# Performance work log

Measured on AMD Instinct MI355X. Metric: run time of the kernel, lower is better.

## Reference

```python
import jax, jax.numpy as jnp
import numpy as np

INPUT_HW = (800, 1024)
STRIDE = 16
HS, WS = INPUT_HW[0] // STRIDE, INPUT_HW[1] // STRIDE  # 50, 64
FG_T, BG_T = 0.7, 0.3
POS_FRAC = 0.5
BATCH_PER_IMG = 256
POS_CAP = int(BATCH_PER_IMG * POS_FRAC)  # 128
# config.anchors: 3 scales x 3 ratios, (w, h) in pixels
_scales = np.array([128.0, 256.0, 512.0])
_ratios = np.array([0.5, 1.0, 2.0])
ANCHOR_WH = np.stack([np.array([s * np.sqrt(r), s / np.sqrt(r)])
                      for s in _scales for r in _ratios], axis=0).astype(np.float32)  # [9,2]
A = ANCHOR_WH.shape[0]
N = HS * WS * A


def build_anchors():
    """Normalized x1y1x2y2 anchors, invalid (out-of-image) anchors zeroed. [N,4]"""
    gx, gy = np.meshgrid(np.arange(WS), np.arange(HS))            # [HS,WS]
    center = (np.stack([gx, gy], -1).astype(np.float32) + 0.5) * STRIDE  # [HS,WS,2]
    center = center[:, :, None, :]                                 # [HS,WS,1,2]
    wh_img = np.array([WS * STRIDE, HS * STRIDE], np.float32)      # (1024, 800)
    a = ANCHOR_WH[None, None, :, :]
    x1y1 = (center - a / 2.0) / wh_img                             # [HS,WS,A,2]
    x2y2 = (center + a / 2.0) / wh_img
    valid = ((x1y1[..., 0] > 0) & (x1y1[..., 1] > 0) &
             (x2y2[..., 0] < 1) & (x2y2[..., 1] < 1)).astype(np.float32)
    boxes = np.concatenate([x1y1, x2y2], -1) * valid[..., None]
    return jnp.asarray(boxes.reshape(N, 4))


def cal_iou(anchors, gt):  # anchors [N,4], gt [M,4] -> [N,M]
    a = anchors[:, None, :]
    g = gt[None, :, :]
    mins = jnp.maximum(a[..., :2], g[..., :2])
    maxs = jnp.minimum(a[..., 2:], g[..., 2:])
    wh = jnp.maximum(maxs - mins, 0.0)
    inter = wh[..., 0] * wh[..., 1]
    area_a = (a[..., 2] - a[..., 0]) * (a[..., 3] - a[..., 1])
    area_g = (g[..., 2] - g[..., 0]) * (g[..., 3] - g[..., 1])
    return inter / (area_a + area_g - inter + 1e-7)


def encode_offset(gt, ref):  # [N,4], [N,4] -> [N,4] tx,ty,tw,th
    w_gt = gt[:, 2] - gt[:, 0]
    h_gt = gt[:, 3] - gt[:, 1]
    xc_gt = (gt[:, 2] + gt[:, 0]) / 2
    yc_gt = (gt[:, 3] + gt[:, 1]) / 2
    w_r = ref[:, 2] - ref[:, 0]
    h_r = ref[:, 3] - ref[:, 1]
    xc_r = (ref[:, 2] + ref[:, 0]) / 2
    yc_r = (ref[:, 3] + ref[:, 1]) / 2
    w_rs = jnp.where(w_r > 0, w_r, 1.0)  # guard zeroed (invalid) anchors
    h_rs = jnp.where(h_r > 0, h_r, 1.0)
    tx = jnp.where(w_gt > 0, (xc_gt - xc_r) / w_rs, 0.0)
    ty = jnp.where(h_gt > 0, (yc_gt - yc_r) / h_rs, 0.0)
    tw = jnp.where(w_gt > 0, jnp.log(jnp.where(w_gt > 0, w_gt / w_rs, 1.0)), 0.0)
    th = jnp.where(h_gt > 0, jnp.log(jnp.where(h_gt > 0, h_gt / h_rs, 1.0)), 0.0)
    return jnp.stack([tx, ty, tw, th], -1)


def _per_image(gt, key, anchors):
    iou = cal_iou(anchors, gt)                    # [N,M]
    matched_iou = iou.max(axis=-1)                # [N]
    matched_idx = iou.argmax(axis=-1)             # [N]
    best_iou = iou.max(axis=0)                    # [M]
    best_idx = iou.argmax(axis=0)                 # [M]
    # positive candidates: high-IoU anchors + per-gt best-matching anchors
    forced = jnp.zeros((N,), jnp.float32).at[best_idx].max(
        jnp.where(best_iou > 0, 1.0, 0.0))
    pos_cand = (matched_iou > FG_T) | (forced > 0)
    neg_cand = matched_iou < BG_T
    n_pos = jnp.minimum(pos_cand.sum(), POS_CAP)
    n_neg = BATCH_PER_IMG - n_pos
    k1, k2 = jax.random.split(key)
    # random subsampling: random priority + rank threshold == random_shuffle[:n]
    rp = jnp.where(pos_cand, jax.random.uniform(k1, (N,)), -1.0)
    rank_p = jnp.argsort(jnp.argsort(-rp))
    sel_pos = pos_cand & (rank_p < n_pos)
    rn = jnp.where(neg_cand, jax.random.uniform(k2, (N,)), -1.0)
    rank_n = jnp.argsort(jnp.argsort(-rn))
    sel_neg = neg_cand & (rank_n < n_neg)
    # offsets for sampled positives against their matched gt
    offsets = encode_offset(gt[matched_idx], anchors)          # [N,4]
    offsets = offsets * sel_pos[:, None].astype(offsets.dtype)
    cls = -jnp.ones((N,), jnp.float32)
    cls = jnp.where(sel_pos, 1.0, cls)
    cls = jnp.where(sel_neg, 0.0, cls)  # neg overwrites, as in the original
    return jnp.concatenate([cls[:, None], offsets], axis=-1)   # [N,5]


def setup_inputs() -> dict:
    key = jax.random.key(0)
    B, M, C = 16, 64, 20
    k1, k2, k3 = jax.random.split(key, 3)
    xy1 = jax.random.uniform(k1, (B, M, 2)) * 0.7
    wh = jax.random.uniform(k2, (B, M, 2)) * 0.25 + 0.02
    boxes = jnp.concatenate([xy1, jnp.minimum(xy1 + wh, 1.0)], axis=-1)
    cls_part = jax.random.uniform(k3, (B, M, C + 1))
    x = jnp.concatenate([cls_part, boxes], axis=-1).astype(jnp.float32)  # [B,M,25]
    return {"x": x}


def reference(x) -> jnp.ndarray:
    gt = x[..., -4:]                      # [B,M,4]
    B = gt.shape[0]
    anchors = build_anchors()             # [N,4]
    keys = jax.random.split(jax.random.key(42), B)
    out = jax.vmap(lambda g, k: _per_image(g, k, anchors))(gt, keys)  # [B,N,5]
    return out.reshape(B, HS, WS, A, 1 + 4)
```

## Files before the change

### kernel.cpp

```cpp
#include <hip/hip_runtime.h>
#include <stdint.h>
#include <math.h>

typedef unsigned int u32;
typedef unsigned long long u64;

#define NN_ 28800
#define MM_ 64
#define BB_ 16
#define XROW_ 25
#define POS_CAP_ 128u
#define BATCH_ 256u
#define NBLK_ 75
#define XSPAN_ 1579

struct Keys { u32 k[BB_][4]; };

__host__ __device__ __forceinline__ u32 rotl32(u32 v, u32 r){ return (v<<r)|(v>>(32u-r)); }

__host__ __device__ __forceinline__ void tf2x32(u32 k0, u32 k1, u32 x0, u32 x1, u32& y0, u32& y1){
  u32 ks2 = k0 ^ k1 ^ 0x1BD11BDAu;
  x0 += k0; x1 += k1;
#define TFR(r) { x0 += x1; x1 = rotl32(x1,(r)); x1 ^= x0; }
  TFR(13) TFR(15) TFR(26) TFR(6)   x0 += k1;  x1 += ks2 + 1u;
  TFR(17) TFR(29) TFR(16) TFR(24)  x0 += ks2; x1 += k0  + 2u;
  TFR(13) TFR(15) TFR(26) TFR(6)   x0 += k0;  x1 += k1  + 3u;
  TFR(17) TFR(29) TFR(16) TFR(24)  x0 += k1;  x1 += ks2 + 4u;
  TFR(13) TFR(15) TFR(26) TFR(6)   x0 += ks2; x1 += k0  + 5u;
#undef TFR
  y0 = x0; y1 = x1;
}

__device__ __forceinline__ void anchor_from(int a, int cell,
                                            float& ox1, float& oy1, float& ox2, float& oy2){
  #pragma clang fp contract(off)
  int w = cell & 63;
  int h = cell >> 6;
  int p = (a >= 6) ? 2 : ((a >= 3) ? 1 : 0);
  int q = a - p*3;
  float sf = (p==0) ? 128.0f : ((p==1) ? 256.0f : 512.0f);
  const float SQH = 0.70710678118654752440f;
  const float SQ2 = 1.41421356237309514547f;
  float cw = (q==0) ? SQH : ((q==1) ? 1.0f : SQ2);
  float ch = (q==0) ? SQ2 : ((q==1) ? 1.0f : SQH);
  float hx = (sf*cw) * 0.5f;
  float hy = (sf*ch) * 0.5f;
  float cx = ((float)w + 0.5f) * 16.0f;
  float cy = ((float)h + 0.5f) * 16.0f;
  float X1 = (cx - hx) / 1024.0f;
  float Y1 = (cy - hy) / 800.0f;
  float X2 = (cx + hx) / 1024.0f;
  float Y2 = (cy + hy) / 800.0f;
  bool valid = (X1 > 0.0f) && (Y1 > 0.0f) && (X2 < 1.0f) && (Y2 < 1.0f);
  ox1 = valid ? X1 : 0.0f;
  oy1 = valid ? Y1 : 0.0f;
  ox2 = valid ? X2 : 0.0f;
  oy2 = valid ? Y2 : 0.0f;
}

__device__ __forceinline__ float rdlane(float v, int k){
  return __int_as_float(__builtin_amdgcn_readlane(__float_as_int(v), k));
}

__device__ __forceinline__ float iou_of(float bx1,float by1,float bx2,float by2,float ba,
                                        float gx1,float gy1,float gx2,float gy2,float garea){
  #pragma clang fp contract(off)
  float ix1 = fmaxf(bx1,gx1), iy1 = fmaxf(by1,gy1);
  float ix2 = fminf(bx2,gx2), iy2 = fminf(by2,gy2);
  float iw = fmaxf(ix2-ix1, 0.0f), ih = fmaxf(iy2-iy1, 0.0f);
  float inter = iw*ih;
  float den = ba + garea;
  den = den - inter;
  den = den + 1e-7f;
  return inter / den;
}

__global__ __launch_bounds__(384) void k_main(const float* __restrict__ x, Keys keys,
                                              u64* __restrict__ bestpart,
                                              u32* __restrict__ cnts_part,
                                              u32* __restrict__ rpv, u32* __restrict__ rnv){
  #pragma clang fp contract(off)
  int tid = threadIdx.x;
  int lane = tid & 63;
  int wid = tid >> 6;
  int bx = blockIdx.x;
  int b = blockIdx.y;
  int cbase = (bx*6 + wid)*64;

  __shared__ float xr[XSPAN_];
  for (int t = tid; t < XSPAN_; t += 384) xr[t] = x[b*(MM_*XROW_) + 21 + t];
  __syncthreads();

  float gx1 = xr[25*lane+0], gy1 = xr[25*lane+1], gx2 = xr[25*lane+2], gy2 = xr[25*lane+3];
  float garea = (gx2-gx1)*(gy2-gy1);

  int ia = cbase + lane;
  int a = ia % 9, cell = ia / 9;
  float ax1,ay1,ax2,ay2;
  anchor_from(a, cell, ax1,ay1,ax2,ay2);
  float aarea = (ax2-ax1)*(ay2-ay1);

  u64 valid_mask = __ballot(ax2 > 0.0f);
  u64 pcbits = 0;
  u64 ncbits = ~valid_mask;
  u64 bk = 0;

  u64 vm = valid_mask;
  while (vm){
    int k1 = __ffsll((unsigned long long)vm) - 1; vm &= vm - 1ull;
    int k2 = vm ? __ffsll((unsigned long long)vm) - 1 : k1; vm &= vm - 1ull;
    int k3 = vm ? __ffsll((unsigned long long)vm) - 1 : k1; vm &= vm - 1ull;
    int k4 = vm ? __ffsll((unsigned long long)vm) - 1 : k1; vm &= vm - 1ull;
    float c1x1=rdlane(ax1,k1), c1y1=rdlane(ay1,k1), c1x2=rdlane(ax2,k1), c1y2=rdlane(ay2,k1), c1a=rdlane(aarea,k1);
    float c2x1=rdlane(ax1,k2), c2y1=rdlane(ay1,k2), c2x2=rdlane(ax2,k2), c2y2=rdlane(ay2,k2), c2a=rdlane(aarea,k2);
    float c3x1=rdlane(ax1,k3), c3y1=rdlane(ay1,k3), c3x2=rdlane(ax2,k3), c3y2=rdlane(ay2,k3), c3a=rdlane(aarea,k3);
    float c4x1=rdlane(ax1,k4), c4y1=rdlane(ay1,k4), c4x2=rdlane(ax2,k4), c4y2=rdlane(ay2,k4), c4a=rdlane(aarea,k4);
    float i1 = iou_of(c1x1,c1y1,c1x2,c1y2,c1a, gx1,gy1,gx2,gy2,garea);
    float i2 = iou_of(c2x1,c2y1,c2x2,c2y2,c2a, gx1,gy1,gx2,gy2,garea);
    float i3 = iou_of(c3x1,c3y1,c3x2,c3y2,c3a, gx1,gy1,gx2,gy2,garea);
    float i4 = iou_of(c4x1,c4y1,c4x2,c4y2,c4a, gx1,gy1,gx2,gy2,garea);
    u64 p1 = __ballot(i1 > 0.7f), n1 = __ballot(i1 >= 0.3f);
    u64 p2 = __ballot(i2 > 0.7f), n2 = __ballot(i2 >= 0.3f);
    u64 p3 = __ballot(i3 > 0.7f), n3 = __ballot(i3 >= 0.3f);
    u64 p4 = __ballot(i4 > 0.7f), n4 = __ballot(i4 >= 0.3f);
    if (p1)  pcbits |= 1ull << k1;
    if (!n1) ncbits |= 1ull << k1;
    if (p2)  pcbits |= 1ull << k2;
    if (!n2) ncbits |= 1ull << k2;
    if (p3)  pcbits |= 1ull << k3;
    if (!n3) ncbits |= 1ull << k3;
    if (p4)  pcbits |= 1ull << k4;
    if (!n4) ncbits |= 1ull << k4;
    u32 q1 = __float_as_uint(i1), q2 = __float_as_uint(i2);
    u32 q3 = __float_as_uint(i3), q4 = __float_as_uint(i4);
    u64 key1 = ((u64)q1 << 32) | (u64)(0xFFFFFFFFu - (u32)(cbase + k1));
    u64 key2 = ((u64)q2 << 32) | (u64)(0xFFFFFFFFu - (u32)(cbase + k2));
    u64 key3 = ((u64)q3 << 32) | (u64)(0xFFFFFFFFu - (u32)(cbase + k3));
    u64 key4 = ((u64)q4 << 32) | (u64)(0xFFFFFFFFu - (u32)(cbase + k4));
    if (q1 && key1 > bk) bk = key1;
    if (q2 && key2 > bk) bk = key2;
    if (q3 && key3 > bk) bk = key3;
    if (q4 && key4 > bk) bk = key4;
  }

  int i = cbase + lane;
  bool pc = (pcbits >> lane) & 1ull;
  bool nc = (ncbits >> lane) & 1ull;
  u32 rp = 0, rn = 0;
  if (pcbits){
    u32 a0,a1;
    tf2x32(keys.k[b][0], keys.k[b][1], 0u, (u32)i, a0,a1);
    rp = pc ? ((a0^a1) >> 9) + 1u : 0u;
  }
  if (ncbits){
    u32 c0,c1;
    tf2x32(keys.k[b][2], keys.k[b][3], 0u, (u32)i, c0,c1);
    rn = nc ? ((c0^c1) >> 9) + 1u : 0u;
  }
  rpv[b*NN_+i] = rp;
  rnv[b*NN_+i] = rn;

  __shared__ u64 wl[384];
  __shared__ u32 scnt[12];
  wl[wid*64 + lane] = bk;
  if (lane == 0){
    scnt[wid*2+0] = (u32)__popcll(pcbits);
    scnt[wid*2+1] = (u32)__popcll(ncbits);
  }
  __syncthreads();
  if (tid < 64){
    u64 m = wl[tid];
    #pragma unroll
    for (int w = 1; w < 6; ++w){ u64 v = wl[w*64+tid]; if (v > m) m = v; }
    bestpart[((size_t)(b*NBLK_ + bx))*64 + tid] = m;
  }
  if (tid == 0){
    u32 c0 = 0, c1 = 0;
    #pragma unroll
    for (int w = 0; w < 6; ++w){ c0 += scnt[w*2+0]; c1 += scnt[w*2+1]; }
    cnts_part[(b*NBLK_ + bx)*2 + 0] = c0;
    cnts_part[(b*NBLK_ + bx)*2 + 1] = c1;
  }
}

__global__ __launch_bounds__(1024) void k_selfix(const float* __restrict__ x,
                                                 const u64* __restrict__ bestpart,
                                                 const u32* __restrict__ cnts_part,
                                                 Keys keys,
                                                 u32* __restrict__ rpv,
                                                 const u32* __restrict__ rnv,
                                                 u32* __restrict__ selp){
  #pragma clang fp contract(off)
  int cls = blockIdx.x, b = blockIdx.y, tid = threadIdx.x;
  int lane = tid & 63, wid = tid >> 6;
  int id = b*2 + cls;

  __shared__ float gbox[MM_][4];
  __shared__ float ga[MM_];
  __shared__ u64 red[16][64];
  __shared__ u32 scp[16], scn[16];
  __shared__ u32 fist[64];
  __shared__ float fmx[16][64];
  __shared__ u32 sq[4];
  __shared__ u32 hist[4096];
  __shared__ u32 wt[16], wsuf[16];
  __shared__ u32 bc[2];
  __shared__ u64 L[512];
  __shared__ u32 lc;

  if (tid < 256) gbox[tid>>2][tid&3] = x[(b*MM_ + (tid>>2))*XROW_ + 21 + (tid&3)];
  __syncthreads();
  if (tid < MM_){
    float g0=gbox[tid][0], g1=gbox[tid][1], g2=gbox[tid][2], g3=gbox[tid][3];
    ga[tid] = (g2-g0)*(g3-g1);
  }

  u64 m = 0;
  for (int blk = wid; blk < NBLK_; blk += 16){
    u64 v = bestpart[((size_t)(b*NBLK_ + blk))*64 + lane];
    if (v > m) m = v;
  }
  red[wid][lane] = m;

  u32 cp = 0, cn = 0;
  if (tid < NBLK_){ cp = cnts_part[(b*NBLK_+tid)*2+0]; cn = cnts_part[(b*NBLK_+tid)*2+1]; }
  #pragma unroll
  for (int off = 32; off >= 1; off >>= 1){
    cp += (u32)__shfl_xor((int)cp, off, 64);
    cn += (u32)__shfl_xor((int)cn, off, 64);
  }
  if (lane == 0){ scp[wid] = cp; scn[wid] = cn; }
  __syncthreads();

  if (tid < 64){
    u64 mm = red[0][tid];
    #pragma unroll
    for (int w = 1; w < 16; ++w){ u64 v = red[w][tid]; if (v > mm) mm = v; }
    fist[tid] = ((u32)(mm >> 32) != 0u) ? (0xFFFFFFFFu - (u32)mm) : 0xFFFFFFFFu;
  }
  if (tid == 0){
    u32 c0 = 0, c1 = 0;
    for (int w = 0; w < 16; ++w){ c0 += scp[w]; c1 += scn[w]; }
    sq[0] = c0; sq[1] = c1;
  }
  __syncthreads();

  {
    int j = tid & 63, q = tid >> 6;
    float mm = 0.0f;
    u32 fi = fist[j];
    if (fi != 0xFFFFFFFFu){
      float ax1,ay1,ax2,ay2;
      anchor_from((int)(fi % 9), (int)(fi / 9), ax1,ay1,ax2,ay2);
      float aarea = (ax2-ax1)*(ay2-ay1);
      #pragma unroll
      for (int t = 0; t < 4; ++t){
        int j2 = q*4 + t;
        float iou = iou_of(ax1,ay1,ax2,ay2,aarea,
                           gbox[j2][0],gbox[j2][1],gbox[j2][2],gbox[j2][3], ga[j2]);
        mm = fmaxf(mm, iou);
      }
    }
    fmx[q][j] = mm;
  }
  __syncthreads();

  if (tid < 64){
    int j = tid;
    u32 fi = fist[j];
    bool valid = (fi != 0xFFFFFFFFu);
    float mm = fmx[0][j];
    #pragma unroll
    for (int q = 1; q < 16; ++q) mm = fmaxf(mm, fmx[q][j]);
    bool wasc = (mm > 0.7f);
    bool first = true;
    for (int j2 = 0; j2 < j; ++j2) if (fist[j2] == fi) first = false;
    bool add = valid && !wasc && first;
    u64 bal = __ballot(add);
    if (cls == 0 && valid){
      u32 a0,a1; tf2x32(keys.k[b][0], keys.k[b][1], 0u, fi, a0,a1);
      rpv[(size_t)b*NN_ + fi] = ((a0^a1) >> 9) + 1u;
    }
    if (tid == 0) sq[2] = sq[0] + (u32)__popcll(bal);
  }
  __syncthreads();

  u32 posc = sq[2], negc = sq[1];
  u32 npos = min(posc, POS_CAP_);
  u32 K   = cls ? (BATCH_ - npos) : npos;
  u32 cnt = cls ? negc : posc;
  if (cnt <= K){
    if (tid == 0){ selp[id*2+0] = 0u; selp[id*2+1] = 0xFFFFFFFFu; }
    return;
  }

  const u32* v = (cls ? rnv : rpv) + (size_t)b*NN_;
  const uint4* v4 = (const uint4*)v;
  #pragma unroll
  for (int h = 0; h < 4; ++h) hist[h*1024 + tid] = 0;
  if (tid == 0) lc = 0;
  __syncthreads();
  for (int i2 = tid; i2 < NN_/4; i2 += 1024){
    uint4 q = v4[i2];
    if (q.x) atomicAdd(&hist[(q.x-1u)>>11], 1u);
    if (q.y) atomicAdd(&hist[(q.y-1u)>>11], 1u);
    if (q.z) atomicAdd(&hist[(q.z-1u)>>11], 1u);
    if (q.w) atomicAdd(&hist[(q.w-1u)>>11], 1u);
  }
  __syncthreads();
  u32 s = hist[tid*4+0] + hist[tid*4+1] + hist[tid*4+2] + hist[tid*4+3];
  u32 incl = s;
  #pragma unroll
  for (int off = 1; off < 64; off <<= 1){
    u32 o = (u32)__shfl_down((int)incl, off, 64);
    incl += (lane + off < 64) ? o : 0u;
  }
  if (lane == 0) wt[wid] = incl;
  __syncthreads();
  if (tid < 16){ u32 ss = 0; for (int w = tid+1; w < 16; ++w) ss += wt[w]; wsuf[tid] = ss; }
  __syncthreads();
  u32 excl = incl - s + wsuf[wid];
  if (excl < K && excl + s >= K){
    u32 acc = excl;
    for (int q = 3; q >= 0; --q){
      u32 h = hist[tid*4 + q];
      if (acc + h >= K){ bc[0] = (u32)(tid*4 + q); bc[1] = K - acc; break; }
      acc += h;
    }
  }
  __syncthreads();
  u32 B = bc[0], Kp = bc[1];
  for (int i2 = tid; i2 < NN_/4; i2 += 1024){
    uint4 q = v4[i2];
    #pragma unroll
    for (int c = 0; c < 4; ++c){
      u32 xv = (c==0)?q.x:(c==1)?q.y:(c==2)?q.z:q.w;
      if (xv && ((xv - 1u) >> 11) == B){
        u32 p = atomicAdd(&lc, 1u);
        if (p < 512u) L[p] = ((u64)xv << 32) | (u32)(i2*4 + c);
      }
    }
  }
  __syncthreads();
  u32 n = min(lc, 512u);
  if (tid < (int)n){
    u64 me = L[tid]; u32 mv = (u32)(me >> 32), mi = (u32)me;
    u32 r = 0;
    for (u32 t2 = 0; t2 < n; ++t2){
      u64 o = L[t2]; u32 ov = (u32)(o >> 32), oi = (u32)o;
      r += (ov > mv) || (ov == mv && oi < mi);
    }
    if (r == Kp - 1u){ selp[id*2+0] = mv; selp[id*2+1] = mi; }
  }
}

__global__ __launch_bounds__(256) void k_out(const float* __restrict__ x,
                                             const u32* __restrict__ rpv,
                                             const u32* __restrict__ rnv,
                                             const u32* __restrict__ selp,
                                             float* __restrict__ out){
  #pragma clang fp contract(off)
  int b = blockIdx.y, tid = threadIdx.x;
  __shared__ float xr[XSPAN_];
  for (int t = tid; t < XSPAN_; t += 256) xr[t] = x[b*(MM_*XROW_) + 21 + t];
  __syncthreads();
  int i = blockIdx.x*256 + tid;
  if (i >= NN_) return;

  u32 pth = selp[(b*2+0)*2+0], pcut = selp[(b*2+0)*2+1];
  u32 nth = selp[(b*2+1)*2+0], ncut = selp[(b*2+1)*2+1];
  u32 pv = rpv[b*NN_+i], nv = rnv[b*NN_+i];
  bool selpos = (pv > 0u) && (pv > pth || (pv == pth && (u32)i <= pcut));
  bool selneg = (nv > 0u) && (nv > nth || (nv == nth && (u32)i <= ncut));
  float cls = selpos ? 1.0f : -1.0f;
  if (selneg) cls = 0.0f;

  float tx = 0.0f, ty = 0.0f, tw = 0.0f, th = 0.0f;
  if (selpos){
    int a = i % 9, cell = i / 9;
    float ax1,ay1,ax2,ay2;
    anchor_from(a, cell, ax1,ay1,ax2,ay2);
    float area_a = (ax2-ax1)*(ay2-ay1);
    float best = -1.0f; int bj = 0;
    for (int j = 0; j < MM_; ++j){
      float g0=xr[25*j+0], g1=xr[25*j+1], g2=xr[25*j+2], g3=xr[25*j+3];
      float ix1 = fmaxf(ax1,g0), iy1 = fmaxf(ay1,g1);
      float ix2 = fminf(ax2,g2), iy2 = fminf(ay2,g3);
      float iw = fmaxf(ix2-ix1, 0.0f), ih = fmaxf(iy2-iy1, 0.0f);
      float inter = iw*ih;
      float den = area_a + (g2-g0)*(g3-g1);
      den = den - inter;
      den = den + 1e-7f;
      float iou = inter / den;
      if (iou > best){ best = iou; bj = j; }
    }
    float g0=xr[25*bj+0], g1=xr[25*bj+1], g2=xr[25*bj+2], g3=xr[25*bj+3];
    float wgt = g2-g0, hgt = g3-g1;
    float xcg = (g2+g0)*0.5f, ycg = (g3+g1)*0.5f;
    float wr = ax2-ax1, hr = ay2-ay1;
    float xcr = (ax2+ax1)*0.5f, ycr = (ay2+ay1)*0.5f;
    float wrs = (wr > 0.0f) ? wr : 1.0f;
    float hrs = (hr > 0.0f) ? hr : 1.0f;
    tx = (wgt > 0.0f) ? (xcg - xcr)/wrs : 0.0f;
    ty = (hgt > 0.0f) ? (ycg - ycr)/hrs : 0.0f;
    tw = (wgt > 0.0f) ? logf(wgt/wrs) : 0.0f;
    th = (hgt > 0.0f) ? logf(hgt/hrs) : 0.0f;
  }
  float* o = out + (size_t)(b*NN_+i)*5;
  o[0] = cls; o[1] = tx; o[2] = ty; o[3] = tw; o[4] = th;
}

extern "C" void kernel_launch(void* const* d_in, const int* in_sizes, int n_in,
                              void* d_out, int out_size, void* d_ws, size_t ws_size,
                              hipStream_t stream) {
  const float* x = (const float*)d_in[0];
  float* out = (float*)d_out;
  char* ws = (char*)d_ws;

  u32* selp      = (u32*)(ws + 0);
  u64* bestpart  = (u64*)(ws + 512);
  u32* cnts_part = (u32*)(ws + 614912);
  u32* rpv       = (u32*)(ws + 624640);
  u32* rnv       = (u32*)(ws + 2467840);
  (void)ws_size; (void)in_sizes; (void)n_in; (void)out_size;

  Keys keys;
  for (int b = 0; b < BB_; ++b){
    u32 r0, r1;
    tf2x32(0u, 42u, 0u, (u32)b, r0, r1);
    tf2x32(r0, r1, 0u, 0u, keys.k[b][0], keys.k[b][1]);
    tf2x32(r0, r1, 0u, 1u, keys.k[b][2], keys.k[b][3]);
  }

  k_main  <<<dim3(NBLK_, BB_), 384, 0, stream>>>(x, keys, bestpart, cnts_part, rpv, rnv);
  k_selfix<<<dim3(2, BB_), 1024, 0, stream>>>(x, bestpart, cnts_part, keys, rpv, rnv, selp);
  k_out   <<<dim3(113, BB_), 256, 0, stream>>>(x, rpv, rnv, selp, out);
}
```

Before: 71.14 us.

## Restructure anchor IoU pass into valid-row blocks with row-level early skip

The main kernel now splits its work into two kinds of blocks. Sixteen blocks per image walk only the valid anchor rows, grouped per anchor shape, using per-shape geometry ranges computed on the host. A wave skips the whole row when no ground-truth box overlaps it vertically. The other blocks only fill in random values for invalid anchors and count them. This removes the per-anchor readlane broadcasts and any IoU work on invalid anchors, and it shrinks the best-key reduction in k_selfix. The cost is load imbalance across the row blocks and more complex indexing.

```diff
diff --git a/kernel.cpp b/kernel.cpp
--- a/kernel.cpp
+++ b/kernel.cpp
@@ -11,10 +11,13 @@
 #define XROW_ 25
 #define POS_CAP_ 128u
 #define BATCH_ 256u
-#define NBLK_ 75
 #define XSPAN_ 1579
+#define RBLK_ 16
+#define FBLK_ 75
+#define NPART_ (RBLK_ + FBLK_)
 
 struct Keys { u32 k[BB_][4]; };
+struct Geo  { int wlo[9], wspan[9], hlo[9], rowbase[10]; float hxv[9], hyv[9]; };
 
 __host__ __device__ __forceinline__ u32 rotl32(u32 v, u32 r){ return (v<<r)|(v>>(32u-r)); }
 
@@ -31,11 +34,7 @@
   y0 = x0; y1 = x1;
 }
 
-__device__ __forceinline__ void anchor_from(int a, int cell,
-                                            float& ox1, float& oy1, float& ox2, float& oy2){
-  #pragma clang fp contract(off)
-  int w = cell & 63;
-  int h = cell >> 6;
+__host__ __device__ __forceinline__ void anchor_hxy(int a, float& hx, float& hy){
   int p = (a >= 6) ? 2 : ((a >= 3) ? 1 : 0);
   int q = a - p*3;
   float sf = (p==0) ? 128.0f : ((p==1) ? 256.0f : 512.0f);
@@ -43,8 +42,16 @@
   const float SQ2 = 1.41421356237309514547f;
   float cw = (q==0) ? SQH : ((q==1) ? 1.0f : SQ2);
   float ch = (q==0) ? SQ2 : ((q==1) ? 1.0f : SQH);
-  float hx = (sf*cw) * 0.5f;
-  float hy = (sf*ch) * 0.5f;
+  hx = (sf*cw) * 0.5f;
+  hy = (sf*ch) * 0.5f;
+}
+
+__device__ __forceinline__ void anchor_from(int a, int cell,
+                                            float& ox1, float& oy1, float& ox2, float& oy2){
+  #pragma clang fp contract(off)
+  int w = cell & 63;
+  int h = cell >> 6;
+  float hx, hy; anchor_hxy(a, hx, hy);
   float cx = ((float)w + 0.5f) * 16.0f;
   float cy = ((float)h + 0.5f) * 16.0f;
   float X1 = (cx - hx) / 1024.0f;
@@ -58,10 +65,6 @@
   oy2 = valid ? Y2 : 0.0f;
 }
 
-__device__ __forceinline__ float rdlane(float v, int k){
-  return __int_as_float(__builtin_amdgcn_readlane(__float_as_int(v), k));
-}
-
 __device__ __forceinline__ float iou_of(float bx1,float by1,float bx2,float by2,float ba,
                                         float gx1,float gy1,float gx2,float gy2,float garea){
   #pragma clang fp contract(off)
@@ -75,7 +78,7 @@
   return inter / den;
 }
 
-__global__ __launch_bounds__(384) void k_main(const float* __restrict__ x, Keys keys,
+__global__ __launch_bounds__(384) void k_main(const float* __restrict__ x, Keys keys, Geo geo,
                                               u64* __restrict__ bestpart,
                                               u32* __restrict__ cnts_part,
                                               u32* __restrict__ rpv, u32* __restrict__ rnv){
@@ -85,101 +88,121 @@
   int wid = tid >> 6;
   int bx = blockIdx.x;
   int b = blockIdx.y;
-  int cbase = (bx*6 + wid)*64;
-
-  __shared__ float xr[XSPAN_];
-  for (int t = tid; t < XSPAN_; t += 384) xr[t] = x[b*(MM_*XROW_) + 21 + t];
-  __syncthreads();
-
-  float gx1 = xr[25*lane+0], gy1 = xr[25*lane+1], gx2 = xr[25*lane+2], gy2 = xr[25*lane+3];
-  float garea = (gx2-gx1)*(gy2-gy1);
-
-  int ia = cbase + lane;
-  int a = ia % 9, cell = ia / 9;
-  float ax1,ay1,ax2,ay2;
-  anchor_from(a, cell, ax1,ay1,ax2,ay2);
-  float aarea = (ax2-ax1)*(ay2-ay1);
-
-  u64 valid_mask = __ballot(ax2 > 0.0f);
-  u64 pcbits = 0;
-  u64 ncbits = ~valid_mask;
-  u64 bk = 0;
-
-  u64 vm = valid_mask;
-  while (vm){
-    int k1 = __ffsll((unsigned long long)vm) - 1; vm &= vm - 1ull;
-    int k2 = vm ? __ffsll((unsigned long long)vm) - 1 : k1; vm &= vm - 1ull;
-    int k3 = vm ? __ffsll((unsigned long long)vm) - 1 : k1; vm &= vm - 1ull;
-    int k4 = vm ? __ffsll((unsigned long long)vm) - 1 : k1; vm &= vm - 1ull;
-    float c1x1=rdlane(ax1,k1), c1y1=rdlane(ay1,k1), c1x2=rdlane(ax2,k1), c1y2=rdlane(ay2,k1), c1a=rdlane(aarea,k1);
-    float c2x1=rdlane(ax1,k2), c2y1=rdlane(ay1,k2), c2x2=rdlane(ax2,k2), c2y2=rdlane(ay2,k2), c2a=rdlane(aarea,k2);
-    float c3x1=rdlane(ax1,k3), c3y1=rdlane(ay1,k3), c3x2=rdlane(ax2,k3), c3y2=rdlane(ay2,k3), c3a=rdlane(aarea,k3);
-    float c4x1=rdlane(ax1,k4), c4y1=rdlane(ay1,k4), c4x2=rdlane(ax2,k4), c4y2=rdlane(ay2,k4), c4a=rdlane(aarea,k4);
-    float i1 = iou_of(c1x1,c1y1,c1x2,c1y2,c1a, gx1,gy1,gx2,gy2,garea);
-    float i2 = iou_of(c2x1,c2y1,c2x2,c2y2,c2a, gx1,gy1,gx2,gy2,garea);
-    float i3 = iou_of(c3x1,c3y1,c3x2,c3y2,c3a, gx1,gy1,gx2,gy2,garea);
-    float i4 = iou_of(c4x1,c4y1,c4x2,c4y2,c4a, gx1,gy1,gx2,gy2,garea);
-    u64 p1 = __ballot(i1 > 0.7f), n1 = __ballot(i1 >= 0.3f);
-    u64 p2 = __ballot(i2 > 0.7f), n2 = __ballot(i2 >= 0.3f);
-    u64 p3 = __ballot(i3 > 0.7f), n3 = __ballot(i3 >= 0.3f);
-    u64 p4 = __ballot(i4 > 0.7f), n4 = __ballot(i4 >= 0.3f);
-    if (p1)  pcbits |= 1ull << k1;
-    if (!n1) ncbits |= 1ull << k1;
-    if (p2)  pcbits |= 1ull << k2;
-    if (!n2) ncbits |= 1ull << k2;
-    if (p3)  pcbits |= 1ull << k3;
-    if (!n3) ncbits |= 1ull << k3;
-    if (p4)  pcbits |= 1ull << k4;
-    if (!n4) ncbits |= 1ull << k4;
-    u32 q1 = __float_as_uint(i1), q2 = __float_as_uint(i2);
-    u32 q3 = __float_as_uint(i3), q4 = __float_as_uint(i4);
-    u64 key1 = ((u64)q1 << 32) | (u64)(0xFFFFFFFFu - (u32)(cbase + k1));
-    u64 key2 = ((u64)q2 << 32) | (u64)(0xFFFFFFFFu - (u32)(cbase + k2));
-    u64 key3 = ((u64)q3 << 32) | (u64)(0xFFFFFFFFu - (u32)(cbase + k3));
-    u64 key4 = ((u64)q4 << 32) | (u64)(0xFFFFFFFFu - (u32)(cbase + k4));
-    if (q1 && key1 > bk) bk = key1;
-    if (q2 && key2 > bk) bk = key2;
-    if (q3 && key3 > bk) bk = key3;
-    if (q4 && key4 > bk) bk = key4;
-  }
-
-  int i = cbase + lane;
-  bool pc = (pcbits >> lane) & 1ull;
-  bool nc = (ncbits >> lane) & 1ull;
-  u32 rp = 0, rn = 0;
-  if (pcbits){
-    u32 a0,a1;
-    tf2x32(keys.k[b][0], keys.k[b][1], 0u, (u32)i, a0,a1);
-    rp = pc ? ((a0^a1) >> 9) + 1u : 0u;
-  }
-  if (ncbits){
-    u32 c0,c1;
-    tf2x32(keys.k[b][2], keys.k[b][3], 0u, (u32)i, c0,c1);
-    rn = nc ? ((c0^c1) >> 9) + 1u : 0u;
-  }
-  rpv[b*NN_+i] = rp;
-  rnv[b*NN_+i] = rn;
-
-  __shared__ u64 wl[384];
-  __shared__ u32 scnt[12];
-  wl[wid*64 + lane] = bk;
-  if (lane == 0){
-    scnt[wid*2+0] = (u32)__popcll(pcbits);
-    scnt[wid*2+1] = (u32)__popcll(ncbits);
-  }
-  __syncthreads();
-  if (tid < 64){
-    u64 m = wl[tid];
-    #pragma unroll
-    for (int w = 1; w < 6; ++w){ u64 v = wl[w*64+tid]; if (v > m) m = v; }
-    bestpart[((size_t)(b*NBLK_ + bx))*64 + tid] = m;
-  }
-  if (tid == 0){
-    u32 c0 = 0, c1 = 0;
-    #pragma unroll
-    for (int w = 0; w < 6; ++w){ c0 += scnt[w*2+0]; c1 += scnt[w*2+1]; }
-    cnts_part[(b*NBLK_ + bx)*2 + 0] = c0;
-    cnts_part[(b*NBLK_ + bx)*2 + 1] = c1;
+
+  if (bx < RBLK_){
+    __shared__ float xr[XSPAN_];
+    for (int t = tid; t < XSPAN_; t += 384) xr[t] = x[b*(MM_*XROW_) + 21 + t];
+    __syncthreads();
+    float gx1 = xr[25*lane+0], gy1 = xr[25*lane+1], gx2 = xr[25*lane+2], gy2 = xr[25*lane+3];
+    float garea = (gx2-gx1)*(gy2-gy1);
+
+    int nrows = geo.rowbase[9];
+    u32 cp = 0, cn = 0;
+    u64 bk = 0;
+
+    for (int rr = 0; rr < 3; ++rr){
+      int r = bx*18 + wid*3 + rr;
+      if (r >= nrows) break;
+      int a = 0;
+      #pragma unroll 8
+      for (int t = 0; t < 8; ++t) if (r >= geo.rowbase[a+1]) ++a;
+      int h = geo.hlo[a] + (r - geo.rowbase[a]);
+      float hx = geo.hxv[a], hy = geo.hyv[a];
+      float cy = ((float)h + 0.5f)*16.0f;
+      float ay1 = (cy - hy)/800.0f, ay2 = (cy + hy)/800.0f;
+      float dy = ay2 - ay1;
+      float iy1 = fmaxf(ay1, gy1), iy2 = fminf(ay2, gy2);
+      float ihj = fmaxf(iy2 - iy1, 0.0f);
+      int wlo = geo.wlo[a], wspan = geo.wspan[a];
+      u64 fullm = (wspan >= 64) ? ~0ull : ((1ull << wspan) - 1ull);
+      u64 pcm = 0, ncm = 0;
+      if (__ballot(ihj != 0.0f) == 0ull){
+        ncm = fullm;
+      } else {
+        #pragma unroll 2
+        for (int k = 0; k < wspan; ++k){
+          float cx = ((float)(wlo + k) + 0.5f)*16.0f;
+          float bx1 = (cx - hx)/1024.0f, bx2 = (cx + hx)/1024.0f;
+          float ix1 = fmaxf(bx1, gx1), ix2 = fminf(bx2, gx2);
+          float iw = fmaxf(ix2 - ix1, 0.0f);
+          float inter = iw * ihj;
+          float areaa = (bx2 - bx1)*dy;
+          float den = areaa + garea;
+          den = den - inter;
+          den = den + 1e-7f;
+          float iou = inter / den;
+          u64 pcb = __ballot(iou > 0.7f);
+          u64 ncb = __ballot(iou >= 0.3f);
+          if (pcb)  pcm |= 1ull << k;
+          if (!ncb) ncm |= 1ull << k;
+          u32 ib = __float_as_uint(iou);
+          if (ib){
+            int i = (h*64 + wlo + k)*9 + a;
+            u64 key = ((u64)ib << 32) | (u64)(0xFFFFFFFFu - (u32)i);
+            if (key > bk) bk = key;
+          }
+        }
+      }
+      if (lane < wspan){
+        int i = (h*64 + wlo + lane)*9 + a;
+        bool pcL = (pcm >> lane) & 1ull;
+        bool ncL = (ncm >> lane) & 1ull;
+        u32 rp = 0, rn = 0;
+        if (pcm){
+          u32 a0,a1; tf2x32(keys.k[b][0], keys.k[b][1], 0u, (u32)i, a0,a1);
+          rp = pcL ? ((a0^a1) >> 9) + 1u : 0u;
+        }
+        if (ncm){
+          u32 c0,c1; tf2x32(keys.k[b][2], keys.k[b][3], 0u, (u32)i, c0,c1);
+          rn = ncL ? ((c0^c1) >> 9) + 1u : 0u;
+        }
+        rpv[(size_t)b*NN_ + i] = rp;
+        rnv[(size_t)b*NN_ + i] = rn;
+      }
+      cp += (u32)__popcll(pcm);
+      cn += (u32)__popcll(ncm);
+    }
+
+    __shared__ u64 wl[384];
+    __shared__ u32 scnt[12];
+    wl[wid*64 + lane] = bk;
+    if (lane == 0){ scnt[wid*2+0] = cp; scnt[wid*2+1] = cn; }
+    __syncthreads();
+    if (tid < 64){
+      u64 m = wl[tid];
+      #pragma unroll
+      for (int w = 1; w < 6; ++w){ u64 v = wl[w*64+tid]; if (v > m) m = v; }
+      bestpart[((size_t)(b*RBLK_ + bx))*64 + tid] = m;
+    }
+    if (tid == 0){
+      u32 c0 = 0, c1 = 0;
+      #pragma unroll
+      for (int w = 0; w < 6; ++w){ c0 += scnt[w*2+0]; c1 += scnt[w*2+1]; }
+      cnts_part[(b*NPART_ + bx)*2 + 0] = c0;
+      cnts_part[(b*NPART_ + bx)*2 + 1] = c1;
+    }
+  } else {
+    int i = (bx - RBLK_)*384 + tid;
+    int a = i % 9, cell = i / 9;
+    float ax1,ay1,ax2,ay2;
+    anchor_from(a, cell, ax1,ay1,ax2,ay2);
+    bool inv = !(ax2 > 0.0f);
+    if (inv){
+      u32 c0,c1; tf2x32(keys.k[b][2], keys.k[b][3], 0u, (u32)i, c0,c1);
+      rpv[(size_t)b*NN_ + i] = 0u;
+      rnv[(size_t)b*NN_ + i] = ((c0^c1) >> 9) + 1u;
+    }
+    __shared__ u32 scnt2[6];
+    u64 bal = __ballot(inv);
+    if (lane == 0) scnt2[wid] = (u32)__popcll(bal);
+    __syncthreads();
+    if (tid == 0){
+      u32 c1 = 0;
+      #pragma unroll
+      for (int w = 0; w < 6; ++w) c1 += scnt2[w];
+      cnts_part[(b*NPART_ + bx)*2 + 0] = 0u;
+      cnts_part[(b*NPART_ + bx)*2 + 1] = c1;
+    }
   }
 }
 
@@ -215,15 +238,10 @@
     ga[tid] = (g2-g0)*(g3-g1);
   }
 
-  u64 m = 0;
-  for (int blk = wid; blk < NBLK_; blk += 16){
-    u64 v = bestpart[((size_t)(b*NBLK_ + blk))*64 + lane];
-    if (v > m) m = v;
-  }
-  red[wid][lane] = m;
+  red[wid][lane] = bestpart[((size_t)(b*RBLK_ + wid))*64 + lane];
 
   u32 cp = 0, cn = 0;
-  if (tid < NBLK_){ cp = cnts_part[(b*NBLK_+tid)*2+0]; cn = cnts_part[(b*NBLK_+tid)*2+1]; }
+  if (tid < NPART_){ cp = cnts_part[(b*NPART_+tid)*2+0]; cn = cnts_part[(b*NPART_+tid)*2+1]; }
   #pragma unroll
   for (int off = 32; off >= 1; off >>= 1){
     cp += (u32)__shfl_xor((int)cp, off, 64);
@@ -369,7 +387,7 @@
 
   u32 pth = selp[(b*2+0)*2+0], pcut = selp[(b*2+0)*2+1];
   u32 nth = selp[(b*2+1)*2+0], ncut = selp[(b*2+1)*2+1];
-  u32 pv = rpv[b*NN_+i], nv = rnv[b*NN_+i];
+  u32 pv = rpv[(size_t)b*NN_+i], nv = rnv[(size_t)b*NN_+i];
   bool selpos = (pv > 0u) && (pv > pth || (pv == pth && (u32)i <= pcut));
   bool selneg = (nv > 0u) && (nv > nth || (nv == nth && (u32)i <= ncut));
   float cls = selpos ? 1.0f : -1.0f;
@@ -406,7 +424,7 @@
     tw = (wgt > 0.0f) ? logf(wgt/wrs) : 0.0f;
     th = (hgt > 0.0f) ? logf(hgt/hrs) : 0.0f;
   }
-  float* o = out + (size_t)(b*NN_+i)*5;
+  float* o = out + (size_t)((size_t)b*NN_+i)*5;
   o[0] = cls; o[1] = tx; o[2] = ty; o[3] = tw; o[4] = th;
 }
 
@@ -419,9 +437,9 @@
 
   u32* selp      = (u32*)(ws + 0);
   u64* bestpart  = (u64*)(ws + 512);
-  u32* cnts_part = (u32*)(ws + 614912);
-  u32* rpv       = (u32*)(ws + 624640);
-  u32* rnv       = (u32*)(ws + 2467840);
+  u32* cnts_part = (u32*)(ws + 131584);
+  u32* rpv       = (u32*)(ws + 143360);
+  u32* rnv       = (u32*)(ws + 1986560);
   (void)ws_size; (void)in_sizes; (void)n_in; (void)out_size;
 
   Keys keys;
@@ -432,7 +450,31 @@
     tf2x32(r0, r1, 0u, 1u, keys.k[b][2], keys.k[b][3]);
   }
 
-  k_main  <<<dim3(NBLK_, BB_), 384, 0, stream>>>(x, keys, bestpart, cnts_part, rpv, rnv);
+  Geo geo;
+  int rb = 0;
+  for (int a = 0; a < 9; ++a){
+    float hx, hy; anchor_hxy(a, hx, hy);
+    int wlo = 64, whi = -1;
+    for (int w = 0; w < 64; ++w){
+      float cx = ((float)w + 0.5f)*16.0f;
+      float X1 = (cx - hx)/1024.0f, X2 = (cx + hx)/1024.0f;
+      if (X1 > 0.0f && X2 < 1.0f){ if (w < wlo) wlo = w; if (w > whi) whi = w; }
+    }
+    int hlo = 50, hhi = -1;
+    for (int h = 0; h < 50; ++h){
+      float cy = ((float)h + 0.5f)*16.0f;
+      float Y1 = (cy - hy)/800.0f, Y2 = (cy + hy)/800.0f;
+      if (Y1 > 0.0f && Y2 < 1.0f){ if (h < hlo) hlo = h; if (h > hhi) hhi = h; }
+    }
+    geo.wlo[a] = wlo; geo.wspan[a] = (whi >= wlo) ? (whi - wlo + 1) : 0;
+    geo.hlo[a] = hlo;
+    geo.hxv[a] = hx;  geo.hyv[a] = hy;
+    geo.rowbase[a] = rb;
+    rb += (hhi >= hlo && whi >= wlo) ? (hhi - hlo + 1) : 0;
+  }
+  geo.rowbase[9] = rb;
+
+  k_main  <<<dim3(NPART_, BB_), 384, 0, stream>>>(x, keys, geo, bestpart, cnts_part, rpv, rnv);
   k_selfix<<<dim3(2, BB_), 1024, 0, stream>>>(x, bestpart, cnts_part, keys, rpv, rnv, selp);
   k_out   <<<dim3(113, BB_), 256, 0, stream>>>(x, rpv, rnv, selp, out);
 }
```

Result: slower. 94.47 us (+32.8%).
